# Performance work log

Hardware: AMD Instinct MI355X
Metric: run time of the kernel (lower is better)

Reference implementation:

```python
import jax, jax.numpy as jnp
import numpy as np

MODEL_DIM = 1024
RANK = 128

def setup_inputs() -> dict:
    key = jax.random.key(0)
    k1, k2 = jax.random.split(key)
    batch = jax.random.normal(k1, (8, 512, MODEL_DIM), dtype=jnp.float32)
    # nn.init.uniform_(proj, -0.05, 0.05)
    proj = jax.random.uniform(k2, (MODEL_DIM, RANK), dtype=jnp.float32, minval=-0.05, maxval=0.05)
    return {"batch": batch, "proj": proj}

def reference(batch, proj):
    # project: (B, S, D) @ (D, R) -> (B, S, R)
    transformed = jnp.matmul(batch, proj)
    # all-pairs squared L2 distance via broadcast diff, matching the torch math
    # diffs: (B, S, S, R)
    diffs = transformed[:, :, None, :] - transformed[:, None, :, :]
    squared_distances = jnp.sum(diffs * diffs, axis=-1)  # (B, S, S)
    return squared_distances
```

## Files before the change

kernel.cpp:

```cpp
#include <hip/hip_runtime.h>

#define SEQ 512
#define MD  1024
#define RK  128

typedef __attribute__((ext_vector_type(8))) short  bf16x8;
typedef __attribute__((ext_vector_type(4))) float  floatx4;
typedef __attribute__((ext_vector_type(4))) unsigned int uint4v;
typedef __attribute__((ext_vector_type(4))) unsigned short ushortx4;

__device__ inline unsigned short f2bf(float f) {
    union { float f; unsigned u; } v; v.f = f;
    unsigned r = v.u + 0x7fffu + ((v.u >> 16) & 1u);
    return (unsigned short)(r >> 16);
}

#define REDW 2112

__global__ __launch_bounds__(512, 2) void proj_direct(
    const float* __restrict__ batch, const float* __restrict__ proj,
    unsigned short* __restrict__ T, float* __restrict__ Nrm)
{
    __shared__ float Red[8 * REDW];

    const int t    = threadIdx.x;
    const int w    = t >> 6;
    const int l    = t & 63;
    const int lm   = l & 15;
    const int quad = l >> 4;
    const int r0   = blockIdx.x * 16;

    floatx4 acc[8];
    #pragma unroll
    for (int i = 0; i < 8; ++i) acc[i] = (floatx4){0.f, 0.f, 0.f, 0.f};

    const float* arow = batch + (size_t)(r0 + lm) * MD + w * 128 + quad * 8;

    #pragma unroll
    for (int s = 0; s < 4; ++s) {
        float4 a0 = *(const float4*)(arow + s * 32);
        float4 a1 = *(const float4*)(arow + s * 32 + 4);
        bf16x8 av;
        av[0] = (short)f2bf(a0.x); av[1] = (short)f2bf(a0.y);
        av[2] = (short)f2bf(a0.z); av[3] = (short)f2bf(a0.w);
        av[4] = (short)f2bf(a1.x); av[5] = (short)f2bf(a1.y);
        av[6] = (short)f2bf(a1.z); av[7] = (short)f2bf(a1.w);

        const float* bk = proj + (size_t)(w * 128 + s * 32 + quad * 8) * RK + lm;
        #pragma unroll
        for (int nt = 0; nt < 8; ++nt) {
            const float* bp = bk + nt * 16;
            bf16x8 bv;
            #pragma unroll
            for (int j = 0; j < 8; ++j)
                bv[j] = (short)f2bf(bp[(size_t)j * RK]);
            acc[nt] = __builtin_amdgcn_mfma_f32_16x16x32_bf16(av, bv, acc[nt], 0, 0, 0);
        }
    }

    #pragma unroll
    for (int nt = 0; nt < 8; ++nt) {
        #pragma unroll
        for (int r = 0; r < 4; ++r) {
            Red[w * REDW + (quad * 4 + r) * 132 + nt * 16 + lm] = acc[nt][r];
        }
    }
    __syncthreads();

    {
        const int row  = t >> 5;
        const int col4 = (t & 31) * 4;
        float4 s4 = {0.f, 0.f, 0.f, 0.f};
        #pragma unroll
        for (int ww = 0; ww < 8; ++ww) {
            float4 p = *(const float4*)(Red + ww * REDW + row * 132 + col4);
            s4.x += p.x; s4.y += p.y; s4.z += p.z; s4.w += p.w;
        }
        unsigned short tmp[4];
        tmp[0] = f2bf(s4.x); tmp[1] = f2bf(s4.y);
        tmp[2] = f2bf(s4.z); tmp[3] = f2bf(s4.w);
        *(ushortx4*)(T + (size_t)(r0 + row) * RK + col4) = *(ushortx4*)tmp;

        float ss = s4.x * s4.x + s4.y * s4.y + s4.z * s4.z + s4.w * s4.w;
        ss += __shfl_xor(ss, 1,  64);
        ss += __shfl_xor(ss, 2,  64);
        ss += __shfl_xor(ss, 4,  64);
        ss += __shfl_xor(ss, 8,  64);
        ss += __shfl_xor(ss, 16, 64);
        if ((t & 31) == 0) Nrm[r0 + row] = ss;
    }
}

#define LDB 136

__global__ __launch_bounds__(256) void dist_mfma(
    const unsigned short* __restrict__ T, const float* __restrict__ Nrm,
    float* __restrict__ out)
{
    __shared__ unsigned short Ti[64 * LDB];
    __shared__ unsigned short Tj[64 * LDB];
    __shared__ float nI[64], nJ[64];

    const int t    = threadIdx.x;
    const int w    = t >> 6;
    const int l    = t & 63;
    const int lm   = l & 15;
    const int quad = l >> 4;
    const int jt = blockIdx.x, it = blockIdx.y, b = blockIdx.z;
    const int i0 = it * 64, j0 = jt * 64;
    const unsigned short* Tb = T + (size_t)b * SEQ * RK;

    {
        int row = t >> 2, kq = (t & 3) * 32;
        const unsigned short* si = Tb + (size_t)(i0 + row) * RK + kq;
        const unsigned short* sj = Tb + (size_t)(j0 + row) * RK + kq;
        #pragma unroll
        for (int q = 0; q < 4; ++q) {
            *(uint4v*)(Ti + row * LDB + kq + q * 8) = *(const uint4v*)(si + q * 8);
            *(uint4v*)(Tj + row * LDB + kq + q * 8) = *(const uint4v*)(sj + q * 8);
        }
        if (t < 64)       nI[t]      = Nrm[(size_t)b * SEQ + i0 + t];
        else if (t < 128) nJ[t - 64] = Nrm[(size_t)b * SEQ + j0 + (t - 64)];
    }
    __syncthreads();

    floatx4 acc[4];
    #pragma unroll
    for (int i = 0; i < 4; ++i) acc[i] = (floatx4){0.f, 0.f, 0.f, 0.f};

    #pragma unroll
    for (int s = 0; s < 4; ++s) {
        bf16x8 av = *(const bf16x8*)(Ti + (w * 16 + lm) * LDB + s * 32 + quad * 8);
        #pragma unroll
        for (int nt = 0; nt < 4; ++nt) {
            bf16x8 bv = *(const bf16x8*)(Tj + (nt * 16 + lm) * LDB + s * 32 + quad * 8);
            acc[nt] = __builtin_amdgcn_mfma_f32_16x16x32_bf16(av, bv, acc[nt], 0, 0, 0);
        }
    }

    float niv[4];
    #pragma unroll
    for (int r = 0; r < 4; ++r) niv[r] = nI[w * 16 + quad * 4 + r];

    float* ob = out + ((size_t)b * SEQ + (i0 + w * 16)) * SEQ + j0;
    #pragma unroll
    for (int nt = 0; nt < 4; ++nt) {
        float njv = nJ[nt * 16 + lm];
        #pragma unroll
        for (int r = 0; r < 4; ++r) {
            ob[(size_t)(quad * 4 + r) * SEQ + nt * 16 + lm] =
                niv[r] + njv - 2.f * acc[nt][r];
        }
    }
}

extern "C" void kernel_launch(void* const* d_in, const int* in_sizes, int n_in,
                              void* d_out, int out_size, void* d_ws, size_t ws_size,
                              hipStream_t stream) {
    const float* batch = (const float*)d_in[0];
    const float* proj  = (const float*)d_in[1];
    float* out = (float*)d_out;

    unsigned short* T   = (unsigned short*)d_ws;
    float*          Nrm = (float*)((char*)d_ws + (1 << 20));

    proj_direct<<<256, 512, 0, stream>>>(batch, proj, T, Nrm);
    dist_mfma<<<dim3(8, 8, 8), 256, 0, stream>>>(T, Nrm, out);
}
```

Measured before the change: 77.15 us.

## Pre-transpose proj to bf16 and split projection across output columns per wave

Adds a small kernel that converts proj to bf16 in transposed (N-major) layout once per call, so the projection kernel reads contiguous bf16x8 B fragments instead of eight strided fp32 loads with per-element conversion. The projection kernel now stages a 16-row bf16 A tile in shared memory and gives each wave a 16-column slice over the full K, which removes the cross-wave K-split reduction through a large shared buffer. It adds an extra kernel launch and the workspace for PT, and each wave now runs a 32-step serial MFMA chain.

```diff
diff --git a/kernel.cpp b/kernel.cpp
--- a/kernel.cpp
+++ b/kernel.cpp
@@ -15,13 +15,27 @@
     return (unsigned short)(r >> 16);
 }
 
-#define REDW 2112
+__global__ __launch_bounds__(256) void proj_t(
+    const float* __restrict__ proj, unsigned short* __restrict__ PT)
+{
+    const int tid = blockIdx.x * 256 + threadIdx.x;
+    const int n   = tid & 127;
+    const int kc  = (tid >> 7) * 8;
+    unsigned short tmp[8];
+    #pragma unroll
+    for (int j = 0; j < 8; ++j)
+        tmp[j] = f2bf(proj[(size_t)(kc + j) * RK + n]);
+    *(bf16x8*)(PT + (size_t)n * MD + kc) = *(bf16x8*)tmp;
+}
 
-__global__ __launch_bounds__(512, 2) void proj_direct(
-    const float* __restrict__ batch, const float* __restrict__ proj,
+#define LDA 1032
+
+__global__ __launch_bounds__(512, 2) void proj_rows(
+    const float* __restrict__ batch, const unsigned short* __restrict__ PT,
     unsigned short* __restrict__ T, float* __restrict__ Nrm)
 {
-    __shared__ float Red[8 * REDW];
+    __shared__ unsigned short As[16 * LDA];
+    __shared__ float Np[8][16];
 
     const int t    = threadIdx.x;
     const int w    = t >> 6;
@@ -30,64 +44,53 @@
     const int quad = l >> 4;
     const int r0   = blockIdx.x * 16;
 
-    floatx4 acc[8];
-    #pragma unroll
-    for (int i = 0; i < 8; ++i) acc[i] = (floatx4){0.f, 0.f, 0.f, 0.f};
-
-    const float* arow = batch + (size_t)(r0 + lm) * MD + w * 128 + quad * 8;
-
-    #pragma unroll
-    for (int s = 0; s < 4; ++s) {
-        float4 a0 = *(const float4*)(arow + s * 32);
-        float4 a1 = *(const float4*)(arow + s * 32 + 4);
-        bf16x8 av;
-        av[0] = (short)f2bf(a0.x); av[1] = (short)f2bf(a0.y);
-        av[2] = (short)f2bf(a0.z); av[3] = (short)f2bf(a0.w);
-        av[4] = (short)f2bf(a1.x); av[5] = (short)f2bf(a1.y);
-        av[6] = (short)f2bf(a1.z); av[7] = (short)f2bf(a1.w);
-
-        const float* bk = proj + (size_t)(w * 128 + s * 32 + quad * 8) * RK + lm;
+    {
+        const int row = t >> 5, kb = (t & 31) * 8;
+        const float* src = batch + (size_t)(r0 + row) * MD + kb;
+        unsigned short* dst = As + row * LDA + kb;
         #pragma unroll
-        for (int nt = 0; nt < 8; ++nt) {
-            const float* bp = bk + nt * 16;
-            bf16x8 bv;
-            #pragma unroll
-            for (int j = 0; j < 8; ++j)
-                bv[j] = (short)f2bf(bp[(size_t)j * RK]);
-            acc[nt] = __builtin_amdgcn_mfma_f32_16x16x32_bf16(av, bv, acc[nt], 0, 0, 0);
-        }
-    }
-
-    #pragma unroll
-    for (int nt = 0; nt < 8; ++nt) {
-        #pragma unroll
-        for (int r = 0; r < 4; ++r) {
-            Red[w * REDW + (quad * 4 + r) * 132 + nt * 16 + lm] = acc[nt][r];
+        for (int c = 0; c < 4; ++c) {
+            float4 f0 = *(const float4*)(src + c * 256);
+            float4 f1 = *(const float4*)(src + c * 256 + 4);
+            unsigned short tmp[8];
+            tmp[0] = f2bf(f0.x); tmp[1] = f2bf(f0.y);
+            tmp[2] = f2bf(f0.z); tmp[3] = f2bf(f0.w);
+            tmp[4] = f2bf(f1.x); tmp[5] = f2bf(f1.y);
+            tmp[6] = f2bf(f1.z); tmp[7] = f2bf(f1.w);
+            *(bf16x8*)(dst + c * 256) = *(bf16x8*)tmp;
         }
     }
     __syncthreads();
 
-    {
-        const int row  = t >> 5;
-        const int col4 = (t & 31) * 4;
-        float4 s4 = {0.f, 0.f, 0.f, 0.f};
+    floatx4 acc = (floatx4){0.f, 0.f, 0.f, 0.f};
+    const unsigned short* aptr = As + lm * LDA + quad * 8;
+    const unsigned short* bptr = PT + (size_t)(w * 16 + lm) * MD + quad * 8;
+
+    #pragma unroll
+    for (int s = 0; s < 32; ++s) {
+        bf16x8 av = *(const bf16x8*)(aptr + s * 32);
+        bf16x8 bv = *(const bf16x8*)(bptr + s * 32);
+        acc = __builtin_amdgcn_mfma_f32_16x16x32_bf16(av, bv, acc, 0, 0, 0);
+    }
+
+    #pragma unroll
+    for (int r = 0; r < 4; ++r) {
+        float v = acc[r];
+        T[(size_t)(r0 + quad * 4 + r) * RK + w * 16 + lm] = f2bf(v);
+        float p = v * v;
+        p += __shfl_xor(p, 1, 64);
+        p += __shfl_xor(p, 2, 64);
+        p += __shfl_xor(p, 4, 64);
+        p += __shfl_xor(p, 8, 64);
+        if (lm == 0) Np[w][quad * 4 + r] = p;
+    }
+    __syncthreads();
+
+    if (t < 16) {
+        float s = 0.f;
         #pragma unroll
-        for (int ww = 0; ww < 8; ++ww) {
-            float4 p = *(const float4*)(Red + ww * REDW + row * 132 + col4);
-            s4.x += p.x; s4.y += p.y; s4.z += p.z; s4.w += p.w;
-        }
-        unsigned short tmp[4];
-        tmp[0] = f2bf(s4.x); tmp[1] = f2bf(s4.y);
-        tmp[2] = f2bf(s4.z); tmp[3] = f2bf(s4.w);
-        *(ushortx4*)(T + (size_t)(r0 + row) * RK + col4) = *(ushortx4*)tmp;
-
-        float ss = s4.x * s4.x + s4.y * s4.y + s4.z * s4.z + s4.w * s4.w;
-        ss += __shfl_xor(ss, 1,  64);
-        ss += __shfl_xor(ss, 2,  64);
-        ss += __shfl_xor(ss, 4,  64);
-        ss += __shfl_xor(ss, 8,  64);
-        ss += __shfl_xor(ss, 16, 64);
-        if ((t & 31) == 0) Nrm[r0 + row] = ss;
+        for (int ww = 0; ww < 8; ++ww) s += Np[ww][t];
+        Nrm[r0 + t] = s;
     }
 }
 
@@ -163,7 +166,9 @@
 
     unsigned short* T   = (unsigned short*)d_ws;
     float*          Nrm = (float*)((char*)d_ws + (1 << 20));
+    unsigned short* PT  = (unsigned short*)((char*)d_ws + (1 << 20) + (1 << 16));
 
-    proj_direct<<<256, 512, 0, stream>>>(batch, proj, T, Nrm);
+    proj_t   <<<64,  256, 0, stream>>>(proj, PT);
+    proj_rows<<<256, 512, 0, stream>>>(batch, PT, T, Nrm);
     dist_mfma<<<dim3(8, 8, 8), 256, 0, stream>>>(T, Nrm, out);
 }
```

New measurement: 78.71 us. +2.0%, slower.
